# Performance work log

Hardware: AMD Instinct MI355X
Metric: run time of the kernel (lower is better)

## Reference

```python
import jax, jax.numpy as jnp
import numpy as np

B, T, C = 16, 4096, 256


def setup_inputs() -> dict:
    key = jax.random.key(0)
    kx, kl = jax.random.split(key)
    x = jax.random.normal(kx, (B, T, C), dtype=jnp.float32)
    lengths = jax.random.randint(kl, (B,), T // 2, T + 1)  # valid lengths per sample
    pool_ranges = lengths  # region to pool over; k <= pool_range guaranteed by layer/total_layers choice
    return {
        "x": x,
        "lengths": lengths,
        "pool_ranges": pool_ranges,
        "top_k": 4,
        "layer": 1,
        "total_layers": 4,
    }


def _pool_one(xb, k, pool_range):
    # xb: [T, C]; keep, per column independently, the k largest values among the
    # first pool_range rows, preserving original row order (torch kmax_pooling).
    Trows, Ccols = xb.shape
    valid = jnp.arange(Trows) < pool_range            # [T]
    vals = jnp.where(valid[:, None], xb, -jnp.inf)    # mask invalid rows to rank last
    order = jnp.argsort(-vals, axis=0)                # descending order per column
    rank = jnp.argsort(order, axis=0)                 # inverse permutation = rank of each row
    keep = (rank < k) & valid[:, None]                # [T, C] which entries survive
    pos = jnp.cumsum(keep.astype(jnp.int32), axis=0) - 1  # compacted output row per column
    idx = jnp.where(keep, pos, Trows)                 # dropped entries -> dummy row Trows
    cols = jnp.arange(Ccols)[None, :]
    out = jnp.zeros((Trows + 1, Ccols), xb.dtype).at[idx, cols].set(
        jnp.where(keep, xb, jnp.zeros((), xb.dtype))
    )
    return out[:-1]                                   # [T, C]; rows >= k are zero padding


def reference(x, lengths, pool_ranges, top_k, layer, total_layers):
    # pool_target = max(top_k, ceil((total_layers - layer)/total_layers * length))
    num = total_layers - layer
    k = jnp.maximum(top_k, (num * lengths + total_layers - 1) // total_layers)
    k = jnp.minimum(k, pool_ranges)  # topk requires k <= available rows
    results = jax.vmap(_pool_one)(x, k, pool_ranges)  # [B, T, C], zero-padded past k_i
    pool_result_ranges = k
    return results, pool_result_ranges
```

## Files before the change

kernel.cpp:

```cpp
#include <hip/hip_runtime.h>
#include <stdint.h>


constexpr int T_ROWS = 4096;
constexpr int C_COLS = 256;
constexpr int NBATCH = 16;
constexpr int SBLOCK = 1024;
constexpr int SWAVES = 16;
constexpr int NCHUNK = 8;
constexpr int CROWS  = 512;
constexpr int CPAD   = 17;
constexpr int EPL    = 64;
constexpr int NSUB   = 2;
constexpr int NGB    = C_COLS / SWAVES;
constexpr int NBLK   = NBATCH * NGB;
constexpr size_t NTOT = (size_t)NBATCH * T_ROWS * C_COLS;

__device__ __forceinline__ int compute_k(const int* lengths, const int* pool_ranges,
                                         const int* p_top_k, const int* p_layer,
                                         const int* p_total, int b, int* pr_out)
{
    int pr = pool_ranges[b];
    pr = pr < 0 ? 0 : (pr > T_ROWS ? T_ROWS : pr);
    const int len   = lengths[b];
    const int top_k = p_top_k[0];
    const int tot   = p_total[0];
    const int num   = tot - p_layer[0];
    int k = (num * len + tot - 1) / tot;
    if (k < top_k) k = top_k;
    if (k > pr)    k = pr;
    *pr_out = pr;
    return k;
}

template<int MODE>
__global__ __launch_bounds__(SBLOCK, 4)
void kmax_select_kernel(const float* __restrict__ x,
                        const int*   __restrict__ lengths,
                        const int*   __restrict__ pool_ranges,
                        const int*   __restrict__ p_top_k,
                        const int*   __restrict__ p_layer,
                        const int*   __restrict__ p_total,
                        float*       __restrict__ out,
                        float*       __restrict__ ws)
{
    __shared__ float    stage[2][CROWS][CPAD];
    __shared__ uint32_t hist[SWAVES][256 * NSUB];

    const int t    = threadIdx.x;
    const int lane = t & 63;
    const int wid  = t >> 6;
    const int bid  = blockIdx.x;
    const int b    = bid >> 4;
    const int cgrp = bid & 15;
    const int c0   = cgrp * 16;
    const int c    = c0 + wid;

    int pr;
    const int k = compute_k(lengths, pool_ranges, p_top_k, p_layer, p_total, b, &pr);

    const int rq = t >> 2;
    const int q  = t & 3;
    const float* xb = x + (size_t)b * T_ROWS * C_COLS + (size_t)c0 + (size_t)(q * 4);
    float4 ga[NCHUNK], gb[NCHUNK];
    #pragma unroll
    for (int ci = 0; ci < NCHUNK; ++ci) {
        ga[ci] = *reinterpret_cast<const float4*>(xb + (size_t)(ci * CROWS + rq) * C_COLS);
        gb[ci] = *reinterpret_cast<const float4*>(xb + (size_t)(ci * CROWS + 256 + rq) * C_COLS);
    }

    uint32_t u[EPL];
    #pragma unroll
    for (int ci = 0; ci < NCHUNK; ++ci) {
        const int buf = ci & 1;
        stage[buf][rq      ][q * 4 + 0] = ga[ci].x;
        stage[buf][rq      ][q * 4 + 1] = ga[ci].y;
        stage[buf][rq      ][q * 4 + 2] = ga[ci].z;
        stage[buf][rq      ][q * 4 + 3] = ga[ci].w;
        stage[buf][rq + 256][q * 4 + 0] = gb[ci].x;
        stage[buf][rq + 256][q * 4 + 1] = gb[ci].y;
        stage[buf][rq + 256][q * 4 + 2] = gb[ci].z;
        stage[buf][rq + 256][q * 4 + 3] = gb[ci].w;
        __syncthreads();
        #pragma unroll
        for (int mm = 0; mm < 8; ++mm) {
            const int m = ci * 8 + mm;
            const uint32_t w = __float_as_uint(stage[buf][mm * 64 + lane][wid]);
            const uint32_t key = w ^ ((w >> 31) ? 0xFFFFFFFFu : 0x80000000u);
            u[m] = ((m * 64 + lane) < pr) ? key : 0u;
            asm("" : "+v"(u[m]));
        }
    }

    uint32_t prefix = 0u, pmask = 0u, rem = (uint32_t)k;
    if (k > 0) {
        for (int pass = 0; pass < 4; ++pass) {
            const int shift = 24 - 8 * pass;
            #pragma unroll
            for (int z = 0; z < (256 * NSUB) / 64; ++z)
                hist[wid][z * 64 + lane] = 0u;
            #pragma unroll
            for (int m = 0; m < EPL; ++m) {
                const uint32_t ui = u[m];
                if ((ui & pmask) == prefix)
                    atomicAdd(&hist[wid][((ui >> shift) & 255u) * NSUB + (lane & (NSUB - 1))], 1u);
            }
            uint32_t c4[4], loc[4], s = 0;
            #pragma unroll
            for (int qq = 0; qq < 4; ++qq) {
                const int bin = 255 - (lane * 4 + qq);
                uint32_t cnt = 0;
                #pragma unroll
                for (int z = 0; z < NSUB; ++z) cnt += hist[wid][bin * NSUB + z];
                c4[qq] = cnt; loc[qq] = s; s += cnt;
            }
            uint32_t incl = s;
            #pragma unroll
            for (int off = 1; off < 64; off <<= 1) {
                const uint32_t nb = __shfl_up(incl, (unsigned)off, 64);
                if (lane >= off) incl += nb;
            }
            const uint32_t gexcl = incl - s;
            uint32_t sel = 0, nrem = 0;
            bool found = false;
            #pragma unroll
            for (int qq = 0; qq < 4; ++qq) {
                const uint32_t sbb = gexcl + loc[qq];
                if (sbb < rem && sbb + c4[qq] >= rem) {
                    sel  = (uint32_t)(255 - (lane * 4 + qq));
                    nrem = rem - sbb;
                    found = true;
                }
            }
            const unsigned long long fm = __ballot(found);
            const int src = __ffsll((unsigned long long)fm) - 1;
            sel  = __shfl(sel,  src, 64);
            nrem = __shfl(nrem, src, 64);
            prefix |= sel << shift;
            pmask  |= 0xFFu << shift;
            rem = nrem;
        }

        const uint32_t th = prefix, tn = rem;
        const unsigned long long ltm = (1ull << lane) - 1ull;
        uint32_t G = 0, E = 0;
        const size_t wsbase  = (size_t)(b * 64 + (c >> 2)) * (size_t)(T_ROWS * 4) + (size_t)(c & 3);
        const size_t outbase = (size_t)b * T_ROWS * C_COLS + (size_t)c;
        #pragma unroll
        for (int m = 0; m < EPL; ++m) {
            const int row = m * 64 + lane;
            const uint32_t ui = u[m];
            const bool v    = row < pr;
            const bool mygt = v && (ui > th);
            const bool myeq = v && (ui == th);
            const unsigned long long gm = __ballot(mygt);
            const unsigned long long em = __ballot(myeq);
            const uint32_t my_g = G + (uint32_t)__popcll(gm & ltm);
            const uint32_t my_e = E + (uint32_t)__popcll(em & ltm);
            if (mygt || (myeq && my_e < tn)) {
                const uint32_t pos  = my_g + (my_e < tn ? my_e : tn);
                const uint32_t bits = ui ^ ((ui >> 31) ? 0x80000000u : 0xFFFFFFFFu);
                if (MODE == 0)
                    ws[wsbase + (size_t)pos * 4] = __uint_as_float(bits);
                else
                    out[outbase + (size_t)pos * C_COLS] = __uint_as_float(bits);
            }
            G += (uint32_t)__popcll(gm);
            E += (uint32_t)__popcll(em);
        }
    }

    if (MODE == 1) {
        const size_t outbase = (size_t)b * T_ROWS * C_COLS + (size_t)c;
        for (int r = k + lane; r < T_ROWS; r += 64)
            out[outbase + (size_t)r * C_COLS] = 0.f;
    }

    if (cgrp == 0 && t == 0)
        out[NTOT + (size_t)b] = (float)k;
}

constexpr int TBLOCK = 256;

__global__ __launch_bounds__(TBLOCK)
void kmax_transpose_kernel(const float* __restrict__ ws,
                           const int*   __restrict__ lengths,
                           const int*   __restrict__ pool_ranges,
                           const int*   __restrict__ p_top_k,
                           const int*   __restrict__ p_layer,
                           const int*   __restrict__ p_total,
                           float*       __restrict__ out)
{
    extern __shared__ float4 tile_s[];

    const int bid  = blockIdx.x;
    const int b    = bid >> 6;
    const int tile = bid & 63;
    const int pos0 = tile * 64;

    int pr;
    const int k = compute_k(lengths, pool_ranges, p_top_k, p_layer, p_total, b, &pr);

    const int t = threadIdx.x;
    const int w = t >> 6;
    const int l = t & 63;
    const float4 z4 = make_float4(0.f, 0.f, 0.f, 0.f);
    float4* out4 = reinterpret_cast<float4*>(out);

    if (pos0 < k) {
        const float4* ws4 = reinterpret_cast<const float4*>(ws);
        #pragma unroll
        for (int cgi = 0; cgi < 16; ++cgi) {
            const int cg = cgi * 4 + w;
            tile_s[cg * 64 + (l ^ cg)] =
                ws4[(size_t)(b * 64 + cg) * T_ROWS + (size_t)(pos0 + l)];
        }
        __syncthreads();
        #pragma unroll
        for (int it = 0; it < 16; ++it) {
            const int idx = it * TBLOCK + t;
            const int row = idx >> 6;
            const int cq  = idx & 63;
            const int pos = pos0 + row;
            const float4 v = (pos < k) ? tile_s[cq * 64 + (row ^ cq)] : z4;
            out4[((size_t)b * T_ROWS + (size_t)pos) * (C_COLS / 4) + (size_t)cq] = v;
        }
    } else {
        #pragma unroll
        for (int it = 0; it < 16; ++it) {
            const int idx = it * TBLOCK + t;
            const int row = idx >> 6;
            const int cq  = idx & 63;
            out4[((size_t)b * T_ROWS + (size_t)(pos0 + row)) * (C_COLS / 4) +
                 (size_t)cq] = z4;
        }
    }
}

extern "C" void kernel_launch(void* const* d_in, const int* in_sizes, int n_in,
                              void* d_out, int out_size, void* d_ws, size_t ws_size,
                              hipStream_t stream)
{
    const float* x            = (const float*)d_in[0];
    const int*   lengths      = (const int*)d_in[1];
    const int*   pool_ranges  = (const int*)d_in[2];
    const int*   top_k        = (const int*)d_in[3];
    const int*   layer        = (const int*)d_in[4];
    const int*   total_layers = (const int*)d_in[5];
    float*       out          = (float*)d_out;
    float*       ws           = (float*)d_ws;

    const size_t ws_need = (size_t)NBATCH * 64 * T_ROWS * 4 * sizeof(float);

    if (ws_size >= ws_need) {
        hipLaunchKernelGGL(kmax_select_kernel<0>, dim3(NBLK), dim3(SBLOCK), 0, stream,
                           x, lengths, pool_ranges, top_k, layer, total_layers, out, ws);
        hipLaunchKernelGGL(kmax_transpose_kernel, dim3(NBATCH * 64), dim3(TBLOCK), 65536, stream,
                           ws, lengths, pool_ranges, top_k, layer, total_layers, out);
    } else {
        hipLaunchKernelGGL(kmax_select_kernel<1>, dim3(NBLK), dim3(SBLOCK), 0, stream,
                           x, lengths, pool_ranges, top_k, layer, total_layers, out, ws);
    }
}
```

Baseline: 92.27 us.

## Split each column across two waves with shared histograms and pipelined loads

Each block now handles 8 columns with two waves per column, each wave owning half the rows (32 keys per lane instead of 64). Histograms are shared by the two waves, double-buffered per pass, and combined after a block barrier. Prefix offsets for the compaction come from a cross-wave reduction. Global loads become a two-deep software pipeline in an interleaved chunk order instead of all loads issued up front. The launch bound doubles to 8 blocks, the block index is swizzled, and zero-fill is spread over all threads. The aim is lower register pressure, higher occupancy and more parallelism, at the cost of extra block-wide barriers and 16-bit packed counts in the reduction.

```diff
diff --git a/kernel.cpp b/kernel.cpp
--- a/kernel.cpp
+++ b/kernel.cpp
@@ -6,13 +6,12 @@
 constexpr int C_COLS = 256;
 constexpr int NBATCH = 16;
 constexpr int SBLOCK = 1024;
-constexpr int SWAVES = 16;
+constexpr int COLS_PB = 8;
+constexpr int CROWS  = 512;
+constexpr int CPAD   = 9;
 constexpr int NCHUNK = 8;
-constexpr int CROWS  = 512;
-constexpr int CPAD   = 17;
-constexpr int EPL    = 64;
-constexpr int NSUB   = 2;
-constexpr int NGB    = C_COLS / SWAVES;
+constexpr int EPL    = 32;
+constexpr int NGB    = C_COLS / COLS_PB;
 constexpr int NBLK   = NBATCH * NGB;
 constexpr size_t NTOT = (size_t)NBATCH * T_ROWS * C_COLS;
 
@@ -34,7 +33,7 @@
 }
 
 template<int MODE>
-__global__ __launch_bounds__(SBLOCK, 4)
+__global__ __launch_bounds__(SBLOCK, 8)
 void kmax_select_kernel(const float* __restrict__ x,
                         const int*   __restrict__ lengths,
                         const int*   __restrict__ pool_ranges,
@@ -45,110 +44,140 @@
                         float*       __restrict__ ws)
 {
     __shared__ float    stage[2][CROWS][CPAD];
-    __shared__ uint32_t hist[SWAVES][256 * NSUB];
+    __shared__ uint32_t hist[2][COLS_PB][2][256];
+    __shared__ uint32_t wtot[COLS_PB];
 
     const int t    = threadIdx.x;
     const int lane = t & 63;
     const int wid  = t >> 6;
+    const int col  = wid >> 1;
+    const int half = wid & 1;
     const int bid  = blockIdx.x;
-    const int b    = bid >> 4;
-    const int cgrp = bid & 15;
-    const int c0   = cgrp * 16;
-    const int c    = c0 + wid;
+    const int lin  = (bid & 7) * (NBLK / 8) + (bid >> 3);
+    const int b    = lin >> 5;
+    const int cgrp = lin & 31;
+    const int c0   = cgrp * COLS_PB;
+    const int c    = c0 + col;
 
     int pr;
     const int k = compute_k(lengths, pool_ranges, p_top_k, p_layer, p_total, b, &pr);
 
-    const int rq = t >> 2;
-    const int q  = t & 3;
+    const int rq = t >> 1;
+    const int q  = t & 1;
     const float* xb = x + (size_t)b * T_ROWS * C_COLS + (size_t)c0 + (size_t)(q * 4);
-    float4 ga[NCHUNK], gb[NCHUNK];
+    const int seq[NCHUNK] = {0, 4, 1, 5, 2, 6, 3, 7};
+
+    uint32_t u[EPL];
+    float4 ld[2];
+    ld[0] = *reinterpret_cast<const float4*>(xb + (size_t)(seq[0] * CROWS + rq) * C_COLS);
+
     #pragma unroll
-    for (int ci = 0; ci < NCHUNK; ++ci) {
-        ga[ci] = *reinterpret_cast<const float4*>(xb + (size_t)(ci * CROWS + rq) * C_COLS);
-        gb[ci] = *reinterpret_cast<const float4*>(xb + (size_t)(ci * CROWS + 256 + rq) * C_COLS);
-    }
-
-    uint32_t u[EPL];
-    #pragma unroll
-    for (int ci = 0; ci < NCHUNK; ++ci) {
-        const int buf = ci & 1;
-        stage[buf][rq      ][q * 4 + 0] = ga[ci].x;
-        stage[buf][rq      ][q * 4 + 1] = ga[ci].y;
-        stage[buf][rq      ][q * 4 + 2] = ga[ci].z;
-        stage[buf][rq      ][q * 4 + 3] = ga[ci].w;
-        stage[buf][rq + 256][q * 4 + 0] = gb[ci].x;
-        stage[buf][rq + 256][q * 4 + 1] = gb[ci].y;
-        stage[buf][rq + 256][q * 4 + 2] = gb[ci].z;
-        stage[buf][rq + 256][q * 4 + 3] = gb[ci].w;
+    for (int s = 0; s < NCHUNK; ++s) {
+        const int ci = seq[s];
+        if (s + 1 < NCHUNK)
+            ld[(s + 1) & 1] = *reinterpret_cast<const float4*>(
+                xb + (size_t)(seq[s + 1] * CROWS + rq) * C_COLS);
+        const float4 v = ld[s & 1];
+        float* srow = &stage[s & 1][rq][0];
+        srow[q * 4 + 0] = v.x;
+        srow[q * 4 + 1] = v.y;
+        srow[q * 4 + 2] = v.z;
+        srow[q * 4 + 3] = v.w;
+        if (s == 0) {
+            uint32_t* hf = &hist[0][0][0][0];
+            #pragma unroll
+            for (int z = 0; z < (2 * COLS_PB * 2 * 256) / SBLOCK; ++z)
+                hf[z * SBLOCK + t] = 0u;
+        }
         __syncthreads();
-        #pragma unroll
-        for (int mm = 0; mm < 8; ++mm) {
-            const int m = ci * 8 + mm;
-            const uint32_t w = __float_as_uint(stage[buf][mm * 64 + lane][wid]);
-            const uint32_t key = w ^ ((w >> 31) ? 0xFFFFFFFFu : 0x80000000u);
-            u[m] = ((m * 64 + lane) < pr) ? key : 0u;
-            asm("" : "+v"(u[m]));
+        if ((ci >> 2) == half) {
+            const int mbase = (ci & 3) * 8;
+            #pragma unroll
+            for (int mm = 0; mm < 8; ++mm) {
+                const int m = mbase + mm;
+                const uint32_t w = __float_as_uint(stage[s & 1][mm * 64 + lane][col]);
+                const uint32_t key = w ^ ((w >> 31) ? 0xFFFFFFFFu : 0x80000000u);
+                u[m] = ((half * 2048 + m * 64 + lane) < pr) ? key : 0u;
+                asm("" : "+v"(u[m]));
+            }
         }
     }
 
     uint32_t prefix = 0u, pmask = 0u, rem = (uint32_t)k;
     if (k > 0) {
+        #pragma unroll
         for (int pass = 0; pass < 4; ++pass) {
             const int shift = 24 - 8 * pass;
-            #pragma unroll
-            for (int z = 0; z < (256 * NSUB) / 64; ++z)
-                hist[wid][z * 64 + lane] = 0u;
+            uint32_t* hp = &hist[pass & 1][col][half][0];
             #pragma unroll
             for (int m = 0; m < EPL; ++m) {
                 const uint32_t ui = u[m];
-                if ((ui & pmask) == prefix)
-                    atomicAdd(&hist[wid][((ui >> shift) & 255u) * NSUB + (lane & (NSUB - 1))], 1u);
-            }
-            uint32_t c4[4], loc[4], s = 0;
+                if ((ui & pmask) == prefix) {
+                    const uint32_t g = 255u - ((ui >> shift) & 255u);
+                    atomicAdd(&hp[(g & 3u) * 64u + (g >> 2)], 1u);
+                }
+            }
+            __syncthreads();
+            uint32_t c4[4], loc[4], ssum = 0;
             #pragma unroll
             for (int qq = 0; qq < 4; ++qq) {
-                const int bin = 255 - (lane * 4 + qq);
-                uint32_t cnt = 0;
-                #pragma unroll
-                for (int z = 0; z < NSUB; ++z) cnt += hist[wid][bin * NSUB + z];
-                c4[qq] = cnt; loc[qq] = s; s += cnt;
-            }
-            uint32_t incl = s;
+                const uint32_t cnt = hist[pass & 1][col][0][qq * 64 + lane]
+                                   + hist[pass & 1][col][1][qq * 64 + lane];
+                c4[qq] = cnt; loc[qq] = ssum; ssum += cnt;
+            }
+            uint32_t incl = ssum;
             #pragma unroll
             for (int off = 1; off < 64; off <<= 1) {
                 const uint32_t nb = __shfl_up(incl, (unsigned)off, 64);
                 if (lane >= off) incl += nb;
             }
-            const uint32_t gexcl = incl - s;
+            const uint32_t gexcl = incl - ssum;
             uint32_t sel = 0, nrem = 0;
             bool found = false;
             #pragma unroll
             for (int qq = 0; qq < 4; ++qq) {
                 const uint32_t sbb = gexcl + loc[qq];
                 if (sbb < rem && sbb + c4[qq] >= rem) {
-                    sel  = (uint32_t)(255 - (lane * 4 + qq));
-                    nrem = rem - sbb;
+                    sel   = 255u - (uint32_t)(lane * 4 + qq);
+                    nrem  = rem - sbb;
                     found = true;
                 }
             }
             const unsigned long long fm = __ballot(found);
-            const int src = __ffsll((unsigned long long)fm) - 1;
+            const int src = __ffsll(fm) - 1;
             sel  = __shfl(sel,  src, 64);
             nrem = __shfl(nrem, src, 64);
             prefix |= sel << shift;
             pmask  |= 0xFFu << shift;
             rem = nrem;
+            if (pass < 3) {
+                uint32_t* hz = &hist[(pass + 1) & 1][col][half][0];
+                hz[lane] = 0u; hz[lane + 64] = 0u; hz[lane + 128] = 0u; hz[lane + 192] = 0u;
+            }
         }
 
         const uint32_t th = prefix, tn = rem;
+        uint32_t gcnt = 0, ecnt = 0;
+        #pragma unroll
+        for (int m = 0; m < EPL; ++m) {
+            const bool v = (half * 2048 + m * 64 + lane) < pr;
+            gcnt += (v && u[m] >  th) ? 1u : 0u;
+            ecnt += (v && u[m] == th) ? 1u : 0u;
+        }
+        uint32_t pk = (gcnt << 16) | ecnt;
+        #pragma unroll
+        for (int off = 32; off >= 1; off >>= 1) pk += __shfl_xor(pk, off, 64);
+        if (half == 0 && lane == 0) wtot[col] = pk;
+        __syncthreads();
+        const uint32_t base = half ? wtot[col] : 0u;
+
+        uint32_t G = base >> 16, E = base & 0xFFFFu;
         const unsigned long long ltm = (1ull << lane) - 1ull;
-        uint32_t G = 0, E = 0;
         const size_t wsbase  = (size_t)(b * 64 + (c >> 2)) * (size_t)(T_ROWS * 4) + (size_t)(c & 3);
         const size_t outbase = (size_t)b * T_ROWS * C_COLS + (size_t)c;
         #pragma unroll
         for (int m = 0; m < EPL; ++m) {
-            const int row = m * 64 + lane;
+            const int row = half * 2048 + m * 64 + lane;
             const uint32_t ui = u[m];
             const bool v    = row < pr;
             const bool mygt = v && (ui > th);
@@ -171,9 +200,9 @@
     }
 
     if (MODE == 1) {
-        const size_t outbase = (size_t)b * T_ROWS * C_COLS + (size_t)c;
-        for (int r = k + lane; r < T_ROWS; r += 64)
-            out[outbase + (size_t)r * C_COLS] = 0.f;
+        const int cl = t & 7;
+        for (int r = k + (t >> 3); r < T_ROWS; r += SBLOCK / 8)
+            out[(size_t)b * T_ROWS * C_COLS + (size_t)r * C_COLS + (size_t)(c0 + cl)] = 0.f;
     }
 
     if (cgrp == 0 && t == 0)
```

Measured after the change: 107.7 us. 1.17x slower.
